# Performance work log

Hardware: AMD Instinct MI355X
Metric: run time of the kernel (lower is better)

## Reference

```python
import jax, jax.numpy as jnp
import numpy as np

HEADS = 16


def setup_inputs() -> dict:
    key = jax.random.key(0)
    k1, k2, k3 = jax.random.split(key, 3)
    B, N, C = 4, 2048, 1024
    x = jax.random.normal(k1, (B, N, C), dtype=jnp.float32)
    w_qkv = jax.random.normal(k2, (C, 3 * C), dtype=jnp.float32) * (C ** -0.5)
    b_qkv = jnp.zeros((3 * C,), dtype=jnp.float32)
    w_out = jax.random.normal(k3, (C, C), dtype=jnp.float32) * (C ** -0.5)
    b_out = jnp.zeros((C,), dtype=jnp.float32)
    return {"x": x, "w_qkv": w_qkv, "b_qkv": b_qkv, "w_out": w_out, "b_out": b_out}


def reference(x, w_qkv, b_qkv, w_out, b_out):
    # Dropout layers act as identity in eval mode.
    B, N, C = x.shape
    H = HEADS
    Dh = C // H
    scale = Dh ** -0.5
    qkv = x @ w_qkv + b_qkv                        # [B, N, 3C]
    qkv = qkv.reshape(B, N, 3, H, Dh)
    q = qkv[:, :, 0].transpose(0, 2, 1, 3)         # [B, H, N, Dh]
    k = qkv[:, :, 1].transpose(0, 2, 1, 3)
    v = qkv[:, :, 2].transpose(0, 2, 1, 3)
    attn = jnp.einsum('bhnd,bhmd->bhnm', q, k) * scale
    attn = jax.nn.softmax(attn, axis=-1)
    out = jnp.einsum('bhnm,bhmd->bhnd', attn, v)   # [B, H, N, Dh]
    out = out.transpose(0, 2, 1, 3).reshape(B, N, C)
    return out @ w_out + b_out
```

## Files before the change

kernel.cpp:

```cpp
#include <hip/hip_runtime.h>

typedef __attribute__((ext_vector_type(8))) short bf16x8;
typedef __attribute__((ext_vector_type(4))) float f32x4;
typedef __attribute__((ext_vector_type(16))) float f32x16;

__device__ __forceinline__ ushort f2bf(float f) {
  union { float f; unsigned u; } v; v.f = f;
  unsigned r = v.u + 0x7fffu + ((v.u >> 16) & 1u);
  return (ushort)(r >> 16);
}

__device__ __forceinline__ float bf2f(ushort u) {
  union { float f; unsigned u; } v; v.u = (unsigned)u << 16;
  return v.f;
}

__device__ __forceinline__ unsigned cvt_pk_bf16(float lo, float hi) {
  unsigned r;
  asm("v_cvt_pk_bf16_f32 %0, %1, %2" : "=v"(r) : "v"(lo), "v"(hi));
  return r;
}

__device__ __forceinline__ void permlane32_swap(unsigned& x, unsigned& y) {
  asm("v_permlane32_swap_b32 %0, %1" : "+v"(x), "+v"(y));
}

__device__ __forceinline__ void gload_lds16(const void* g, void* l) {
  __builtin_amdgcn_global_load_lds(
      (const __attribute__((address_space(1))) void*)g,
      (__attribute__((address_space(3))) void*)l, 16, 0, 0);
}


__global__ void cvt_f32_bf16(const float* __restrict__ s, ushort* __restrict__ d, int n) {
  int i = (blockIdx.x * blockDim.x + threadIdx.x) * 4;
  int stride = gridDim.x * blockDim.x * 4;
  for (; i < n; i += stride) {
    float4 v = *reinterpret_cast<const float4*>(s + i);
    ushort4 o;
    o.x = f2bf(v.x); o.y = f2bf(v.y); o.z = f2bf(v.z); o.w = f2bf(v.w);
    *reinterpret_cast<ushort4*>(d + i) = o;
  }
}

__global__ void transpose_cvt(const float* __restrict__ src, ushort* __restrict__ dst,
                              int R, int C) {
  __shared__ float tile[32][33];
  int c0 = blockIdx.x * 32, r0 = blockIdx.y * 32;
  int tx = threadIdx.x, ty = threadIdx.y;
  #pragma unroll
  for (int i = 0; i < 32; i += 8)
    tile[ty + i][tx] = src[(size_t)(r0 + ty + i) * C + c0 + tx];
  __syncthreads();
  #pragma unroll
  for (int i = 0; i < 32; i += 8)
    dst[(size_t)(c0 + ty + i) * R + r0 + tx] = f2bf(tile[tx][ty + i]);
}


#define GEMM_STAGE(buf, Ap, Bp, kt)                                            \
  {                                                                            \
    _Pragma("unroll")                                                          \
    for (int c_ = 0; c_ < 4; ++c_) {                                           \
      const int qq_ = c_ * 256 + tid;                                          \
      const int row_ = qq_ >> 3;                                               \
      const int so_ = ((qq_ & 7) ^ (row_ & 7)) * 8;                            \
      gload_lds16(Ap + (size_t)(bm + row_) * 1024 + (kt) + so_,                \
                  (char*)sA + (buf) * 16384 + qq_ * 16);                       \
      gload_lds16(Bp + (size_t)(bn + row_) * 1024 + (kt) + so_,                \
                  (char*)sB + (buf) * 16384 + qq_ * 16);                       \
    }                                                                          \
  }

#define GEMM_COMPUTE(buf)                                                      \
  {                                                                            \
    const char* bA_ = (const char*)sA + (buf) * 16384;                         \
    const char* bB_ = (const char*)sB + (buf) * 16384;                         \
    bf16x8 af[4][2], bfr[4][2];                                                \
    _Pragma("unroll")                                                          \
    for (int mi = 0; mi < 4; ++mi) {                                           \
      const int row_ = wr * 64 + mi * 16 + lr;                                 \
      const char* p_ = bA_ + row_ * 128;                                       \
      const int sw_ = (row_ & 7) << 4;                                         \
      af[mi][0] = *(const bf16x8*)(p_ + ((lg * 16) ^ sw_));                    \
      af[mi][1] = *(const bf16x8*)(p_ + ((64 + lg * 16) ^ sw_));               \
    }                                                                          \
    _Pragma("unroll")                                                          \
    for (int ni = 0; ni < 4; ++ni) {                                           \
      const int row_ = wc * 64 + ni * 16 + lr;                                 \
      const char* p_ = bB_ + row_ * 128;                                       \
      const int sw_ = (row_ & 7) << 4;                                         \
      bfr[ni][0] = *(const bf16x8*)(p_ + ((lg * 16) ^ sw_));                   \
      bfr[ni][1] = *(const bf16x8*)(p_ + ((64 + lg * 16) ^ sw_));              \
    }                                                                          \
    _Pragma("unroll")                                                          \
    for (int kk = 0; kk < 2; ++kk)                                             \
      _Pragma("unroll")                                                        \
      for (int mi = 0; mi < 4; ++mi)                                           \
        _Pragma("unroll")                                                      \
        for (int ni = 0; ni < 4; ++ni)                                         \
          acc[mi][ni] = __builtin_amdgcn_mfma_f32_16x16x32_bf16(               \
              af[mi][kk], bfr[ni][kk], acc[mi][ni], 0, 0, 0);                  \
  }

#define GEMM_PIPELINE(Ap, Bp)                                                  \
  GEMM_STAGE(0, Ap, Bp, 0);                                                    \
  asm volatile("s_waitcnt vmcnt(0)" ::: "memory");                             \
  __builtin_amdgcn_s_barrier();                                                \
  __builtin_amdgcn_sched_barrier(0);                                           \
  for (int T = 0; T < 16; ++T) {                                               \
    if (T + 1 < 16) GEMM_STAGE((T + 1) & 1, Ap, Bp, (T + 1) * 64);             \
    GEMM_COMPUTE(T & 1);                                                       \
    asm volatile("s_waitcnt vmcnt(0)" ::: "memory");                           \
    __builtin_amdgcn_s_barrier();                                              \
    __builtin_amdgcn_sched_barrier(0);                                         \
  }

#define GEMM_PROLOG                                                            \
  __shared__ __align__(16) ushort sA[2][128 * 64];                             \
  __shared__ __align__(16) ushort sB[2][128 * 64];                             \
  const int tid = threadIdx.x;                                                 \
  const int lane = tid & 63;                                                   \
  const int w = tid >> 6;                                                      \
  const int wr = w >> 1, wc = w & 1;                                           \
  const int lr = lane & 15, lg = lane >> 4;                                    \
  f32x4 acc[4][4] = {};


__global__ __launch_bounds__(256) void gemm_qk(const ushort* __restrict__ A,
                                               const ushort* __restrict__ Bt,
                                               const float* __restrict__ bias,
                                               ushort* __restrict__ q,
                                               ushort* __restrict__ k) {
  GEMM_PROLOG;
  const int id = blockIdx.x;
  const int xcd = id & 7, j = id >> 3;
  const int by = xcd * 8 + (j & 7);
  const int bx = j >> 3;
  const int bm = by * 128;
  const int bn = bx * 128;

  GEMM_PIPELINE(A, Bt);

  ushort* const dst = (bn < 1024) ? q : k;
  const int cb = bn & 1023;
  #pragma unroll
  for (int mi = 0; mi < 4; ++mi)
    #pragma unroll
    for (int ni = 0; ni < 4; ++ni) {
      const int cq = cb + wc * 64 + ni * 16 + lr;
      const int h = cq >> 6, d = cq & 63;
      const float bb = bias[bn + wc * 64 + ni * 16 + lr];
      #pragma unroll
      for (int r = 0; r < 4; ++r) {
        const int row = bm + wr * 64 + mi * 16 + lg * 4 + r;
        const int b_ = row >> 11, n = row & 2047;
        const int bh = b_ * 16 + h;
        dst[((size_t)bh * 2048 + n) * 64 + d] = f2bf(acc[mi][ni][r] + bb);
      }
    }
}


__global__ __launch_bounds__(256) void gemm_vT(const ushort* __restrict__ A,
                                               const ushort* __restrict__ Bt,
                                               const float* __restrict__ bias,
                                               ushort* __restrict__ vT) {
  GEMM_PROLOG;
  const int id = blockIdx.x;
  const int xcd = id & 7, j = id >> 3;
  const int bnb = xcd * 8 + (j & 7);
  const int bmb = j >> 3;
  const int bm = bmb * 128;
  const int bn = bnb * 128;

  GEMM_PIPELINE(A, Bt);

  const int b_ = bn >> 11, n0 = bn & 2047;
  #pragma unroll
  for (int mi = 0; mi < 4; ++mi)
    #pragma unroll
    for (int ni = 0; ni < 4; ++ni) {
      const int ncol = wc * 64 + ni * 16 + lr;
      #pragma unroll
      for (int r = 0; r < 4; ++r) {
        const int m = wr * 64 + mi * 16 + lg * 4 + r;
        const int vc = bm + m;
        const int h = vc >> 6, d = vc & 63;
        const int bh = b_ * 16 + h;
        const float bb = bias[vc];
        vT[((size_t)bh * 64 + d) * 2048 + n0 + ncol] = f2bf(acc[mi][ni][r] + bb);
      }
    }
}


__global__ __launch_bounds__(256) void gemm_out(const ushort* __restrict__ A,
                                                const ushort* __restrict__ Bt,
                                                const float* __restrict__ bias,
                                                float* __restrict__ out) {
  GEMM_PROLOG;
  const int id = blockIdx.x;
  const int xcd = id & 7, j = id >> 3;
  const int by = xcd * 8 + (j & 7);
  const int bx = j >> 3;
  const int bm = by * 128;
  const int bn = bx * 128;

  GEMM_PIPELINE(A, Bt);

  #pragma unroll
  for (int mi = 0; mi < 4; ++mi)
    #pragma unroll
    for (int ni = 0; ni < 4; ++ni) {
      const int col = bn + wc * 64 + ni * 16 + lr;
      const float bb = bias[col];
      #pragma unroll
      for (int r = 0; r < 4; ++r) {
        const int row = bm + wr * 64 + mi * 16 + lg * 4 + r;
        out[(size_t)row * 1024 + col] = acc[mi][ni][r] + bb;
      }
    }
}


__global__ __launch_bounds__(512, 2) void attn_fwd(const ushort* __restrict__ q,
                                                   const ushort* __restrict__ k,
                                                   const ushort* __restrict__ vT,
                                                   ushort* __restrict__ o) {
  __shared__ __align__(16) ushort sK[2][64 * 64];
  __shared__ __align__(16) ushort sV[2][64 * 64];

  const int tid = threadIdx.x, lane = tid & 63, w = tid >> 6;
  const int id = blockIdx.x;
  const int xcd = id & 7, j = id >> 3;
  const int bh = xcd * 8 + (j & 7);
  const int qx = j >> 3;
  const int qrow0 = qx * 256 + w * 32;

  const ushort* Qb = q + (size_t)bh * 2048 * 64;
  const ushort* Kb = k + (size_t)bh * 2048 * 64;
  const ushort* Vb = vT + (size_t)bh * 64 * 2048;
  const int lq = lane & 31, hi = lane >> 5;

  const int srow = lane >> 3;
  const int ssw = ((lane & 7) ^ srow) * 8;
  const int krow = w * 8 + srow;

  gload_lds16(Kb + (size_t)krow * 64 + ssw, &sK[0][w * 512]);
  gload_lds16(Vb + (size_t)krow * 2048 + 0 + ssw, &sV[0][w * 512]);

  const float qs = 0.125f * 1.44269504f;
  bf16x8 qf[4];
  #pragma unroll
  for (int dk = 0; dk < 4; ++dk) {
    bf16x8 t = *(const bf16x8*)(Qb + (size_t)(qrow0 + lq) * 64 + dk * 16 + hi * 8);
    #pragma unroll
    for (int jj = 0; jj < 8; ++jj)
      t[jj] = (short)f2bf(bf2f((ushort)t[jj]) * qs);
    qf[dk] = t;
  }

  float m_run = -1e30f, l_run = 0.f;
  f32x16 oacc[2] = {};

  for (int t = 0; t < 32; ++t) {
    const int cur = t & 1;
    if (t + 1 < 32) {
      const int kv2 = (t + 1) << 6;
      gload_lds16(Kb + (size_t)(kv2 + krow) * 64 + ssw, &sK[cur ^ 1][w * 512]);
      gload_lds16(Vb + (size_t)krow * 2048 + kv2 + ssw, &sV[cur ^ 1][w * 512]);
      asm volatile("s_waitcnt vmcnt(2)" ::: "memory");
    } else {
      asm volatile("s_waitcnt vmcnt(0)" ::: "memory");
    }
    __builtin_amdgcn_s_barrier();
    __builtin_amdgcn_sched_barrier(0);

    const char* kb_ = (const char*)&sK[cur][0];
    const char* vb_ = (const char*)&sV[cur][0];

    f32x16 S[2] = {};
    __builtin_amdgcn_s_setprio(1);
    #pragma unroll
    for (int kvt = 0; kvt < 2; ++kvt) {
      const int row = kvt * 32 + lq;
      const int rsw = (row & 7) << 4;
      #pragma unroll
      for (int dk = 0; dk < 4; ++dk) {
        bf16x8 kf = *(const bf16x8*)(kb_ + row * 128 + ((dk * 32 + hi * 16) ^ rsw));
        S[kvt] = __builtin_amdgcn_mfma_f32_32x32x16_bf16(kf, qf[dk], S[kvt], 0, 0, 0);
      }
    }
    __builtin_amdgcn_s_setprio(0);

    float mx = S[0][0];
    #pragma unroll
    for (int kvt = 0; kvt < 2; ++kvt)
      #pragma unroll
      for (int r = 0; r < 16; ++r) mx = fmaxf(mx, S[kvt][r]);
    const float rm = fmaxf(mx, __shfl_xor(mx, 32, 64));

    if (!__all(rm <= m_run + 8.f)) {
      const float mnew = fmaxf(m_run, rm);
      const float corr = __builtin_amdgcn_exp2f(m_run - mnew);
      m_run = mnew;
      l_run *= corr;
      float cq[16];
      #pragma unroll
      for (int r = 0; r < 16; ++r)
        cq[r] = __shfl(corr, (r & 3) + 8 * (r >> 2) + 4 * hi, 64);
      #pragma unroll
      for (int dt = 0; dt < 2; ++dt)
        #pragma unroll
        for (int r = 0; r < 16; ++r) oacc[dt][r] *= cq[r];
    }

    float psum = 0.f;
    unsigned pk_[2][8];
    #pragma unroll
    for (int kvt = 0; kvt < 2; ++kvt) {
      float e[16];
      #pragma unroll
      for (int r = 0; r < 16; ++r) {
        e[r] = __builtin_amdgcn_exp2f(S[kvt][r] - m_run);
        psum += e[r];
      }
      #pragma unroll
      for (int g = 0; g < 4; ++g) {
        pk_[kvt][g * 2 + 0] = cvt_pk_bf16(e[4 * g + 0], e[4 * g + 1]);
        pk_[kvt][g * 2 + 1] = cvt_pk_bf16(e[4 * g + 2], e[4 * g + 3]);
      }
    }
    psum += __shfl_xor(psum, 32, 64);
    l_run += psum;

    __builtin_amdgcn_s_setprio(1);
    #pragma unroll
    for (int kvt = 0; kvt < 2; ++kvt)
      #pragma unroll
      for (int cc = 0; cc < 2; ++cc) {
        unsigned x0 = pk_[kvt][4 * cc + 0], x1 = pk_[kvt][4 * cc + 1];
        unsigned y0 = pk_[kvt][4 * cc + 2], y1 = pk_[kvt][4 * cc + 3];
        permlane32_swap(x0, y0);
        permlane32_swap(x1, y1);
        union { unsigned u[4]; bf16x8 v; } Am;
        Am.u[0] = x0; Am.u[1] = x1; Am.u[2] = y0; Am.u[3] = y1;
        const int cg = kvt * 2 + cc;
        #pragma unroll
        for (int dt = 0; dt < 2; ++dt) {
          const int row = dt * 32 + lq;
          bf16x8 vf = *(const bf16x8*)(vb_ + row * 128 + ((cg * 32 + hi * 16) ^ ((row & 7) << 4)));
          oacc[dt] = __builtin_amdgcn_mfma_f32_32x32x16_bf16(Am.v, vf, oacc[dt], 0, 0, 0);
        }
      }
    __builtin_amdgcn_s_setprio(0);
    __builtin_amdgcn_s_barrier();
  }

  const int b_ = bh >> 4, h = bh & 15;
  float lf[16];
  #pragma unroll
  for (int r = 0; r < 16; ++r)
    lf[r] = __builtin_amdgcn_rcpf(__shfl(l_run, (r & 3) + 8 * (r >> 2) + 4 * hi, 64));
  #pragma unroll
  for (int dt = 0; dt < 2; ++dt)
    #pragma unroll
    for (int r = 0; r < 16; ++r) {
      const int n = qrow0 + (r & 3) + 8 * (r >> 2) + 4 * hi;
      o[(((size_t)b_ * 2048 + n) * 16 + h) * 64 + dt * 32 + lq] = f2bf(oacc[dt][r] * lf[r]);
    }
}


extern "C" void kernel_launch(void* const* d_in, const int* in_sizes, int n_in,
                              void* d_out, int out_size, void* d_ws, size_t ws_size,
                              hipStream_t stream) {
  const float* x = (const float*)d_in[0];
  const float* w_qkv = (const float*)d_in[1];
  const float* b_qkv = (const float*)d_in[2];
  const float* w_out = (const float*)d_in[3];
  const float* b_out = (const float*)d_in[4];
  float* out = (float*)d_out;
  char* ws = (char*)d_ws;

  ushort* xb    = (ushort*)(ws);
  ushort* wqkvT = (ushort*)(ws + 16777216);
  ushort* woutT = (ushort*)(ws + 23068672);
  ushort* qb    = (ushort*)(ws + 25165824);
  ushort* kb    = (ushort*)(ws + 41943040);
  ushort* vTb   = (ushort*)(ws + 58720256);
  ushort* attnb = (ushort*)(ws + 75497472);

  cvt_f32_bf16<<<2048, 256, 0, stream>>>(x, xb, 8192 * 1024);
  transpose_cvt<<<dim3(96, 32), dim3(32, 8), 0, stream>>>(w_qkv, wqkvT, 1024, 3072);
  transpose_cvt<<<dim3(32, 32), dim3(32, 8), 0, stream>>>(w_out, woutT, 1024, 1024);
  gemm_qk<<<1024, 256, 0, stream>>>(xb, wqkvT, b_qkv, qb, kb);
  gemm_vT<<<512, 256, 0, stream>>>(wqkvT + 2048 * 1024, xb, b_qkv + 2048, vTb);
  attn_fwd<<<512, 512, 0, stream>>>(qb, kb, vTb, attnb);
  gemm_out<<<512, 256, 0, stream>>>(attnb, woutT, b_out, out);
}
```

Measured before the change: 195.8 us.

## Shrink attention blocks to 4 waves and interleave softmax with PV MFMAs

The attention kernel now uses 256-thread blocks covering 128 query rows, launched as 1024 blocks, with launch bounds allowing 4 blocks per CU. Each thread therefore issues two K/V staging loads per buffer and the wait count is adjusted to match. The row max and row sum are computed with tree reductions, and each exp/pack stage now feeds its PV MFMAs right away instead of buffering both halves, which shortens live ranges and raises ILP. In exchange, each K/V tile is loaded by more blocks, so global/L2 traffic per query row rises.

```diff
diff --git a/kernel.cpp b/kernel.cpp
--- a/kernel.cpp
+++ b/kernel.cpp
@@ -224,7 +224,21 @@
 }
 
 
-__global__ __launch_bounds__(512, 2) void attn_fwd(const ushort* __restrict__ q,
+#define ATTN_STAGE(buf, kvbase)                                                \
+  {                                                                            \
+    _Pragma("unroll")                                                          \
+    for (int c_ = 0; c_ < 2; ++c_) {                                           \
+      const int qq_ = c_ * 256 + tid;                                          \
+      const int row_ = qq_ >> 3;                                               \
+      const int so_ = ((qq_ & 7) ^ (row_ & 7)) * 8;                            \
+      gload_lds16(Kb + (size_t)((kvbase) + row_) * 64 + so_,                   \
+                  (char*)&sK[buf][0] + qq_ * 16);                              \
+      gload_lds16(Vb + (size_t)row_ * 2048 + (kvbase) + so_,                   \
+                  (char*)&sV[buf][0] + qq_ * 16);                              \
+    }                                                                          \
+  }
+
+__global__ __launch_bounds__(256, 4) void attn_fwd(const ushort* __restrict__ q,
                                                    const ushort* __restrict__ k,
                                                    const ushort* __restrict__ vT,
                                                    ushort* __restrict__ o) {
@@ -236,19 +250,14 @@
   const int xcd = id & 7, j = id >> 3;
   const int bh = xcd * 8 + (j & 7);
   const int qx = j >> 3;
-  const int qrow0 = qx * 256 + w * 32;
+  const int qrow0 = qx * 128 + w * 32;
 
   const ushort* Qb = q + (size_t)bh * 2048 * 64;
   const ushort* Kb = k + (size_t)bh * 2048 * 64;
   const ushort* Vb = vT + (size_t)bh * 64 * 2048;
   const int lq = lane & 31, hi = lane >> 5;
 
-  const int srow = lane >> 3;
-  const int ssw = ((lane & 7) ^ srow) * 8;
-  const int krow = w * 8 + srow;
-
-  gload_lds16(Kb + (size_t)krow * 64 + ssw, &sK[0][w * 512]);
-  gload_lds16(Vb + (size_t)krow * 2048 + 0 + ssw, &sV[0][w * 512]);
+  ATTN_STAGE(0, 0);
 
   const float qs = 0.125f * 1.44269504f;
   bf16x8 qf[4];
@@ -267,10 +276,8 @@
   for (int t = 0; t < 32; ++t) {
     const int cur = t & 1;
     if (t + 1 < 32) {
-      const int kv2 = (t + 1) << 6;
-      gload_lds16(Kb + (size_t)(kv2 + krow) * 64 + ssw, &sK[cur ^ 1][w * 512]);
-      gload_lds16(Vb + (size_t)krow * 2048 + kv2 + ssw, &sV[cur ^ 1][w * 512]);
-      asm volatile("s_waitcnt vmcnt(2)" ::: "memory");
+      ATTN_STAGE(cur ^ 1, (t + 1) << 6);
+      asm volatile("s_waitcnt vmcnt(4)" ::: "memory");
     } else {
       asm volatile("s_waitcnt vmcnt(0)" ::: "memory");
     }
@@ -294,12 +301,14 @@
     }
     __builtin_amdgcn_s_setprio(0);
 
-    float mx = S[0][0];
-    #pragma unroll
-    for (int kvt = 0; kvt < 2; ++kvt)
-      #pragma unroll
-      for (int r = 0; r < 16; ++r) mx = fmaxf(mx, S[kvt][r]);
-    const float rm = fmaxf(mx, __shfl_xor(mx, 32, 64));
+    float tm[16];
+    #pragma unroll
+    for (int r = 0; r < 16; ++r) tm[r] = fmaxf(S[0][r], S[1][r]);
+    #pragma unroll
+    for (int sgap = 8; sgap > 0; sgap >>= 1)
+      #pragma unroll
+      for (int r = 0; r < sgap; ++r) tm[r] = fmaxf(tm[r], tm[r + sgap]);
+    const float rm = fmaxf(tm[0], __shfl_xor(tm[0], 32, 64));
 
     if (!__all(rm <= m_run + 8.f)) {
       const float mnew = fmaxf(m_run, rm);
@@ -317,31 +326,32 @@
     }
 
     float psum = 0.f;
-    unsigned pk_[2][8];
     #pragma unroll
     for (int kvt = 0; kvt < 2; ++kvt) {
       float e[16];
       #pragma unroll
-      for (int r = 0; r < 16; ++r) {
+      for (int r = 0; r < 16; ++r)
         e[r] = __builtin_amdgcn_exp2f(S[kvt][r] - m_run);
-        psum += e[r];
-      }
+      unsigned pk_[8];
       #pragma unroll
       for (int g = 0; g < 4; ++g) {
-        pk_[kvt][g * 2 + 0] = cvt_pk_bf16(e[4 * g + 0], e[4 * g + 1]);
-        pk_[kvt][g * 2 + 1] = cvt_pk_bf16(e[4 * g + 2], e[4 * g + 3]);
-      }
-    }
-    psum += __shfl_xor(psum, 32, 64);
-    l_run += psum;
-
-    __builtin_amdgcn_s_setprio(1);
-    #pragma unroll
-    for (int kvt = 0; kvt < 2; ++kvt)
+        pk_[g * 2 + 0] = cvt_pk_bf16(e[4 * g + 0], e[4 * g + 1]);
+        pk_[g * 2 + 1] = cvt_pk_bf16(e[4 * g + 2], e[4 * g + 3]);
+      }
+      float ts[8];
+      #pragma unroll
+      for (int r = 0; r < 8; ++r) ts[r] = e[r] + e[r + 8];
+      #pragma unroll
+      for (int sgap = 4; sgap > 0; sgap >>= 1)
+        #pragma unroll
+        for (int r = 0; r < sgap; ++r) ts[r] += ts[r + sgap];
+      psum += ts[0];
+
+      __builtin_amdgcn_s_setprio(1);
       #pragma unroll
       for (int cc = 0; cc < 2; ++cc) {
-        unsigned x0 = pk_[kvt][4 * cc + 0], x1 = pk_[kvt][4 * cc + 1];
-        unsigned y0 = pk_[kvt][4 * cc + 2], y1 = pk_[kvt][4 * cc + 3];
+        unsigned x0 = pk_[4 * cc + 0], x1 = pk_[4 * cc + 1];
+        unsigned y0 = pk_[4 * cc + 2], y1 = pk_[4 * cc + 3];
         permlane32_swap(x0, y0);
         permlane32_swap(x1, y1);
         union { unsigned u[4]; bf16x8 v; } Am;
@@ -354,7 +364,11 @@
           oacc[dt] = __builtin_amdgcn_mfma_f32_32x32x16_bf16(Am.v, vf, oacc[dt], 0, 0, 0);
         }
       }
-    __builtin_amdgcn_s_setprio(0);
+      __builtin_amdgcn_s_setprio(0);
+    }
+    psum += __shfl_xor(psum, 32, 64);
+    l_run += psum;
+
     __builtin_amdgcn_s_barrier();
   }
 
@@ -397,6 +411,6 @@
   transpose_cvt<<<dim3(32, 32), dim3(32, 8), 0, stream>>>(w_out, woutT, 1024, 1024);
   gemm_qk<<<1024, 256, 0, stream>>>(xb, wqkvT, b_qkv, qb, kb);
   gemm_vT<<<512, 256, 0, stream>>>(wqkvT + 2048 * 1024, xb, b_qkv + 2048, vTb);
-  attn_fwd<<<512, 512, 0, stream>>>(qb, kb, vTb, attnb);
+  attn_fwd<<<1024, 256, 0, stream>>>(qb, kb, vTb, attnb);
   gemm_out<<<512, 256, 0, stream>>>(attnb, woutT, b_out, out);
 }
```

Result: slower. 206.7 us (+5.6%).

## Use 256x256 tiles with ping-pong MFMA scheduling for QK GEMM

Applied to the files above, without the earlier changes.

Rewrites the Q/K projection GEMM to use 256x256 output tiles with 8 waves per block and 256 blocks. LDS reads and global prefetches are interleaved with four barrier-separated MFMA phases that raise wave priority during the matrix ops. The shared GEMM pipeline used by the other GEMMs is reordered to issue the next stage's loads and wait with a partial vmcnt before the barrier, so compute runs after the barrier. The larger tile improves operand reuse and cuts LDS traffic per FLOP, but it also means one block per CU and a grid of only 256 blocks, which can leave CUs idle.

```diff
diff --git a/kernel.cpp b/kernel.cpp
--- a/kernel.cpp
+++ b/kernel.cpp
@@ -58,6 +58,128 @@
 }
 
 
+#define QK_STAGE(Sp, Gp, base, kt)                                             \
+  {                                                                            \
+    _Pragma("unroll")                                                          \
+    for (int c_ = 0; c_ < 4; ++c_) {                                           \
+      const int qq_ = c_ * 512 + tid;                                          \
+      const int row_ = qq_ >> 3;                                               \
+      const int so_ = ((qq_ & 7) ^ (row_ & 7)) * 8;                            \
+      gload_lds16(Gp + (size_t)((base) + row_) * 1024 + (kt) + so_,            \
+                  (char*)Sp + qq_ * 16);                                       \
+    }                                                                          \
+  }
+
+#define QK_LDA(buf, mh)                                                        \
+  {                                                                            \
+    _Pragma("unroll")                                                          \
+    for (int mi = 0; mi < 4; ++mi) {                                           \
+      const int row_ = wm * 128 + (mh) * 64 + mi * 16 + lr;                    \
+      const char* p_ = (const char*)&sA[buf][0] + row_ * 128;                  \
+      const int sw_ = (row_ & 7) << 4;                                         \
+      af[mi][0] = *(const bf16x8*)(p_ + ((lg * 16) ^ sw_));                    \
+      af[mi][1] = *(const bf16x8*)(p_ + ((64 + lg * 16) ^ sw_));               \
+    }                                                                          \
+  }
+
+#define QK_LDB(buf, nh)                                                        \
+  {                                                                            \
+    _Pragma("unroll")                                                          \
+    for (int ni = 0; ni < 2; ++ni) {                                           \
+      const int row_ = wn * 64 + (nh) * 32 + ni * 16 + lr;                     \
+      const char* p_ = (const char*)&sB[buf][0] + row_ * 128;                  \
+      const int sw_ = (row_ & 7) << 4;                                         \
+      bf[ni][0] = *(const bf16x8*)(p_ + ((lg * 16) ^ sw_));                    \
+      bf[ni][1] = *(const bf16x8*)(p_ + ((64 + lg * 16) ^ sw_));               \
+    }                                                                          \
+  }
+
+#define QK_MMQ(mh, nh)                                                         \
+  {                                                                            \
+    _Pragma("unroll")                                                          \
+    for (int kk = 0; kk < 2; ++kk)                                             \
+      _Pragma("unroll")                                                        \
+      for (int mi = 0; mi < 4; ++mi)                                           \
+        _Pragma("unroll")                                                      \
+        for (int ni = 0; ni < 2; ++ni)                                         \
+          acc[mh][mi][nh][ni] = __builtin_amdgcn_mfma_f32_16x16x32_bf16(       \
+              af[mi][kk], bf[ni][kk], acc[mh][mi][nh][ni], 0, 0, 0);           \
+  }
+
+#define QK_SYNC_MMQ(mh, nh)                                                    \
+  __builtin_amdgcn_s_barrier();                                                \
+  asm volatile("s_waitcnt lgkmcnt(0)" ::: "memory");                           \
+  __builtin_amdgcn_sched_barrier(0);                                           \
+  __builtin_amdgcn_s_setprio(1);                                               \
+  QK_MMQ(mh, nh);                                                              \
+  __builtin_amdgcn_s_setprio(0);                                               \
+  __builtin_amdgcn_s_barrier();
+
+__global__ __launch_bounds__(512, 1) void gemm_qk(const ushort* __restrict__ A,
+                                                  const ushort* __restrict__ Bt,
+                                                  const float* __restrict__ bias,
+                                                  ushort* __restrict__ q,
+                                                  ushort* __restrict__ k) {
+  __shared__ __align__(16) ushort sA[2][256 * 64];
+  __shared__ __align__(16) ushort sB[2][256 * 64];
+  const int tid = threadIdx.x, lane = tid & 63, w = tid >> 6;
+  const int wm = w >> 2, wn = w & 3;
+  const int lr = lane & 15, lg = lane >> 4;
+
+  const int id = blockIdx.x;
+  const int xcd = id & 7, j = id >> 3;
+  const int by = xcd * 4 + (j & 3);
+  const int bx = j >> 2;
+  const int bm = by * 256, bn = bx * 256;
+
+  f32x4 acc[2][4][2][2] = {};
+  bf16x8 af[4][2], bf[2][2];
+
+  QK_STAGE(&sA[0][0], A, bm, 0);
+  QK_STAGE(&sB[0][0], Bt, bn, 0);
+  asm volatile("s_waitcnt vmcnt(0)" ::: "memory");
+  __builtin_amdgcn_s_barrier();
+
+  for (int T = 0; T < 16; ++T) {
+    const int cur = T & 1;
+    const bool pf = (T + 1 < 16);
+    QK_LDA(cur, 0); QK_LDB(cur, 0);
+    if (pf) QK_STAGE(&sA[cur ^ 1][0], A, bm, (T + 1) * 64);
+    QK_SYNC_MMQ(0, 0);
+    QK_LDB(cur, 1);
+    if (pf) QK_STAGE(&sB[cur ^ 1][0], Bt, bn, (T + 1) * 64);
+    QK_SYNC_MMQ(0, 1);
+    QK_LDA(cur, 1);
+    QK_SYNC_MMQ(1, 1);
+    QK_LDB(cur, 0);
+    asm volatile("s_waitcnt vmcnt(0)" ::: "memory");
+    QK_SYNC_MMQ(1, 0);
+  }
+
+  ushort* const dst = (bn < 1024) ? q : k;
+  const int cb = bn & 1023;
+  #pragma unroll
+  for (int mh = 0; mh < 2; ++mh)
+    #pragma unroll
+    for (int mi = 0; mi < 4; ++mi)
+      #pragma unroll
+      for (int nh = 0; nh < 2; ++nh)
+        #pragma unroll
+        for (int ni = 0; ni < 2; ++ni) {
+          const int cq = cb + wn * 64 + nh * 32 + ni * 16 + lr;
+          const int h = cq >> 6, d = cq & 63;
+          const float bb = bias[bn + wn * 64 + nh * 32 + ni * 16 + lr];
+          #pragma unroll
+          for (int r = 0; r < 4; ++r) {
+            const int row = bm + wm * 128 + mh * 64 + mi * 16 + lg * 4 + r;
+            const int b_ = row >> 11, n = row & 2047;
+            const int bh = b_ * 16 + h;
+            dst[((size_t)bh * 2048 + n) * 64 + d] = f2bf(acc[mh][mi][nh][ni][r] + bb);
+          }
+        }
+}
+
+
 #define GEMM_STAGE(buf, Ap, Bp, kt)                                            \
   {                                                                            \
     _Pragma("unroll")                                                          \
@@ -105,15 +227,17 @@
 
 #define GEMM_PIPELINE(Ap, Bp)                                                  \
   GEMM_STAGE(0, Ap, Bp, 0);                                                    \
-  asm volatile("s_waitcnt vmcnt(0)" ::: "memory");                             \
-  __builtin_amdgcn_s_barrier();                                                \
-  __builtin_amdgcn_sched_barrier(0);                                           \
   for (int T = 0; T < 16; ++T) {                                               \
-    if (T + 1 < 16) GEMM_STAGE((T + 1) & 1, Ap, Bp, (T + 1) * 64);             \
-    GEMM_COMPUTE(T & 1);                                                       \
-    asm volatile("s_waitcnt vmcnt(0)" ::: "memory");                           \
+    if (T + 1 < 16) {                                                          \
+      GEMM_STAGE((T + 1) & 1, Ap, Bp, (T + 1) * 64);                           \
+      asm volatile("s_waitcnt vmcnt(8)" ::: "memory");                         \
+    } else {                                                                   \
+      asm volatile("s_waitcnt vmcnt(0)" ::: "memory");                         \
+    }                                                                          \
     __builtin_amdgcn_s_barrier();                                              \
     __builtin_amdgcn_sched_barrier(0);                                         \
+    GEMM_COMPUTE(T & 1);                                                       \
+    __builtin_amdgcn_s_barrier();                                              \
   }
 
 #define GEMM_PROLOG                                                            \
@@ -125,41 +249,6 @@
   const int wr = w >> 1, wc = w & 1;                                           \
   const int lr = lane & 15, lg = lane >> 4;                                    \
   f32x4 acc[4][4] = {};
-
-
-__global__ __launch_bounds__(256) void gemm_qk(const ushort* __restrict__ A,
-                                               const ushort* __restrict__ Bt,
-                                               const float* __restrict__ bias,
-                                               ushort* __restrict__ q,
-                                               ushort* __restrict__ k) {
-  GEMM_PROLOG;
-  const int id = blockIdx.x;
-  const int xcd = id & 7, j = id >> 3;
-  const int by = xcd * 8 + (j & 7);
-  const int bx = j >> 3;
-  const int bm = by * 128;
-  const int bn = bx * 128;
-
-  GEMM_PIPELINE(A, Bt);
-
-  ushort* const dst = (bn < 1024) ? q : k;
-  const int cb = bn & 1023;
-  #pragma unroll
-  for (int mi = 0; mi < 4; ++mi)
-    #pragma unroll
-    for (int ni = 0; ni < 4; ++ni) {
-      const int cq = cb + wc * 64 + ni * 16 + lr;
-      const int h = cq >> 6, d = cq & 63;
-      const float bb = bias[bn + wc * 64 + ni * 16 + lr];
-      #pragma unroll
-      for (int r = 0; r < 4; ++r) {
-        const int row = bm + wr * 64 + mi * 16 + lg * 4 + r;
-        const int b_ = row >> 11, n = row & 2047;
-        const int bh = b_ * 16 + h;
-        dst[((size_t)bh * 2048 + n) * 64 + d] = f2bf(acc[mi][ni][r] + bb);
-      }
-    }
-}
 
 
 __global__ __launch_bounds__(256) void gemm_vT(const ushort* __restrict__ A,
@@ -395,7 +484,7 @@
   cvt_f32_bf16<<<2048, 256, 0, stream>>>(x, xb, 8192 * 1024);
   transpose_cvt<<<dim3(96, 32), dim3(32, 8), 0, stream>>>(w_qkv, wqkvT, 1024, 3072);
   transpose_cvt<<<dim3(32, 32), dim3(32, 8), 0, stream>>>(w_out, woutT, 1024, 1024);
-  gemm_qk<<<1024, 256, 0, stream>>>(xb, wqkvT, b_qkv, qb, kb);
+  gemm_qk<<<256, 512, 0, stream>>>(xb, wqkvT, b_qkv, qb, kb);
   gemm_vT<<<512, 256, 0, stream>>>(wqkvT + 2048 * 1024, xb, b_qkv + 2048, vTb);
   attn_fwd<<<512, 512, 0, stream>>>(qb, kb, vTb, attnb);
   gemm_out<<<512, 256, 0, stream>>>(attnb, woutT, b_out, out);
```

Result: faster. 183.0 us (-6.5%).
